# Kernel tuning notes

Measured on AMD Instinct MI355X. Metric: run time of the kernel, lower is better.

The kernel has to match this reference:

```python
import jax, jax.numpy as jnp
import numpy as np

SIGMA = 0.5          # kernel length_scale
SOFTNESS = 1.0       # softmax temperature scaling
B, F, J, M, U = 4096, 512, 16, 64, 512  # batch, feature, num_domains, domain_dim, units


def _gauss(sqdist):
    # ExponentiatedQuadratic with amplitude=1: exp(-||x-y||^2 / (2*sigma^2))
    return jnp.exp(-sqdist / (2.0 * SIGMA * SIGMA))


def setup_inputs() -> dict:
    key = jax.random.key(0)
    k1, k2, k3 = jax.random.split(key, 3)
    h = jax.random.normal(k1, (B, F), dtype=jnp.float32)
    # domain basis: keras RandomNormal() default stddev=0.05
    domains = 0.05 * jax.random.normal(k2, (J, M, F), dtype=jnp.float32)
    # W_domains: GlorotUniform over (M, U)
    limit = np.sqrt(6.0 / (M + U)).astype(np.float32)
    W = jax.random.uniform(k3, (J, M, U), dtype=jnp.float32, minval=-limit, maxval=limit)
    b = jnp.zeros((J, U), dtype=jnp.float32)
    return {"h": h, "domains": domains, "W": W, "b": b}


def reference(h, domains, W, b):
    # ---- kernel matrix between inputs and all domain bases: K[b,j,m] ----
    h2 = jnp.sum(h * h, axis=-1)                      # [B]
    d2 = jnp.sum(domains * domains, axis=-1)          # [J,M]
    cross = jnp.einsum('bf,jmf->bjm', h, domains)     # [B,J,M]
    K_hd = _gauss(h2[:, None, None] + d2[None] - 2.0 * cross)

    # ---- per-domain MMD: k(x,x) - 2*mean_m k(x,d_m) + mean_{m,m'} k(d_m,d_m') ----
    dd = d2[:, :, None] + d2[:, None, :] - 2.0 * jnp.einsum('jmf,jnf->jmn', domains, domains)
    k_dd_mean = jnp.mean(_gauss(dd), axis=(1, 2))     # [J]
    mmd = 1.0 - 2.0 * jnp.mean(K_hd, axis=2) + k_dd_mean[None, :]  # [B,J]

    # softmax over domains of -softness * mmd  -> domain probabilities [B,J]
    prob = jax.nn.softmax(-SOFTNESS * mmd, axis=1)

    # ---- representer outputs per domain: K(h, D_j) @ W_j + b_j ----
    out = jnp.einsum('bjm,jmu->bju', K_hd, W) + b[None]  # [B,J,U]

    # probability-weighted sum over domains
    return jnp.einsum('bj,bju->bu', prob, out)           # [B,U]
```

## Files before the change

kernel.cpp:

```cpp
#include <hip/hip_runtime.h>
#include <math.h>

typedef unsigned short ushort_t;
typedef __attribute__((ext_vector_type(8))) short bf16x8;
typedef __attribute__((ext_vector_type(4))) float f32x4;

#define B_SZ 4096
#define F_SZ 512
#define J_SZ 16
#define M_SZ 64
#define U_SZ 512
#define P_SZ 1024

__device__ __forceinline__ ushort_t f2bf(float f) {
    union { float f; unsigned int u; } v; v.f = f;
    unsigned int r = (v.u + 0x7FFFu + ((v.u >> 16) & 1u)) >> 16;
    return (ushort_t)r;
}

__device__ __forceinline__ void gload_lds16(const void* g, void* l) {
    __builtin_amdgcn_global_load_lds(
        (const __attribute__((address_space(1))) unsigned int*)g,
        (__attribute__((address_space(3))) unsigned int*)l, 16, 0, 0);
}

__global__ __launch_bounds__(256) void prep_kernel(const float* __restrict__ h,
                                                   const float* __restrict__ dom,
                                                   const float* __restrict__ W,
                                                   ushort_t* __restrict__ hbf,
                                                   ushort_t* __restrict__ dombf,
                                                   ushort_t* __restrict__ Wt,
                                                   float* __restrict__ h2,
                                                   float* __restrict__ d2,
                                                   float* __restrict__ Gpart) {
    const int bid = blockIdx.x;
    const int tid = threadIdx.x;

    if (bid < 1024) {
        int b = bid * 4 + (tid >> 6);
        int lane = tid & 63;
        const float4* row = (const float4*)(h + (size_t)b * F_SZ);
        ushort4* orow = (ushort4*)(hbf + (size_t)b * F_SZ);
        float s = 0.f;
        for (int i = lane; i < F_SZ / 4; i += 64) {
            float4 v = row[i];
            s += v.x * v.x + v.y * v.y + v.z * v.z + v.w * v.w;
            ushort4 o; o.x = f2bf(v.x); o.y = f2bf(v.y); o.z = f2bf(v.z); o.w = f2bf(v.w);
            orow[i] = o;
        }
        for (int off = 32; off; off >>= 1) s += __shfl_down(s, off);
        if (lane == 0) h2[b] = s;
    } else if (bid < 1280) {
        int p = (bid - 1024) * 4 + (tid >> 6);
        int lane = tid & 63;
        const float4* row = (const float4*)(dom + (size_t)p * F_SZ);
        ushort4* orow = (ushort4*)(dombf + (size_t)p * F_SZ);
        float s = 0.f;
        for (int i = lane; i < F_SZ / 4; i += 64) {
            float4 v = row[i];
            s += v.x * v.x + v.y * v.y + v.z * v.z + v.w * v.w;
            ushort4 o; o.x = f2bf(v.x); o.y = f2bf(v.y); o.z = f2bf(v.z); o.w = f2bf(v.w);
            orow[i] = o;
        }
        for (int off = 32; off; off >>= 1) s += __shfl_down(s, off);
        if (lane == 0) d2[p] = s;
    } else if (bid < 1344) {
        int idx = bid - 1280;
        int j = idx >> 2, kc = idx & 3;
        const float* base = dom + (size_t)j * M_SZ * F_SZ + kc * 128;
        __shared__ float As[32][68];
        int tx = tid & 15, ty = tid >> 4;
        float c[4][4] = {};
        for (int kk = 0; kk < 128; kk += 32) {
            for (int l = 0; l < 2; ++l) {
                int s = tid + l * 256;
                int r = s >> 3, c4 = (s & 7) << 2;
                float4 v = *(const float4*)&base[(size_t)r * F_SZ + kk + c4];
                As[c4 + 0][r] = v.x; As[c4 + 1][r] = v.y;
                As[c4 + 2][r] = v.z; As[c4 + 3][r] = v.w;
            }
            __syncthreads();
            for (int k = 0; k < 32; ++k) {
                float a[4], bv[4];
                for (int i = 0; i < 4; ++i) a[i] = As[k][ty * 4 + i];
                for (int i = 0; i < 4; ++i) bv[i] = As[k][tx * 4 + i];
                for (int i = 0; i < 4; ++i)
                    for (int l2 = 0; l2 < 4; ++l2) c[i][l2] += a[i] * bv[l2];
            }
            __syncthreads();
        }
        float* gout = Gpart + ((size_t)kc * 16 + j) * 4096;
        for (int i = 0; i < 4; ++i)
            for (int l2 = 0; l2 < 4; ++l2)
                gout[(ty * 4 + i) * 64 + tx * 4 + l2] = c[i][l2];
    } else {
        int idx = bid - 1344;
        int pt = (idx >> 3) * 64, ut = (idx & 7) * 64;
        __shared__ ushort_t T[64][72];
        for (int l = 0; l < 4; ++l) {
            int s = l * 256 + tid;
            int r = s >> 4, c4 = (s & 15) << 2;
            float4 v = *(const float4*)&W[(size_t)(pt + r) * U_SZ + ut + c4];
            T[c4 + 0][r] = f2bf(v.x); T[c4 + 1][r] = f2bf(v.y);
            T[c4 + 2][r] = f2bf(v.z); T[c4 + 3][r] = f2bf(v.w);
        }
        __syncthreads();
        for (int l = 0; l < 4; ++l) {
            int s = l * 256 + tid;
            int r2 = s >> 4, c4 = (s & 15) << 2;
            ushort4 o; o.x = T[r2][c4 + 0]; o.y = T[r2][c4 + 1];
            o.z = T[r2][c4 + 2]; o.w = T[r2][c4 + 3];
            *(ushort4*)&Wt[(size_t)(ut + r2) * P_SZ + pt + c4] = o;
        }
    }
}

__global__ __launch_bounds__(256) void kdd_reduce(const float* __restrict__ Gpart,
                                                  const float* __restrict__ d2,
                                                  float* __restrict__ kdd) {
    int j = blockIdx.x, tid = threadIdx.x;
    __shared__ float sd2[M_SZ];
    __shared__ float red[256];
    if (tid < M_SZ) sd2[tid] = d2[j * M_SZ + tid];
    __syncthreads();
    const float* g0 = Gpart + (size_t)(0 * 16 + j) * 4096;
    const float* g1 = Gpart + (size_t)(1 * 16 + j) * 4096;
    const float* g2 = Gpart + (size_t)(2 * 16 + j) * 4096;
    const float* g3 = Gpart + (size_t)(3 * 16 + j) * 4096;
    float acc = 0.f;
    for (int s = tid; s < 4096; s += 256) {
        float G = g0[s] + g1[s] + g2[s] + g3[s];
        int m = s >> 6, n = s & 63;
        acc += __expf(-2.f * (sd2[m] + sd2[n] - 2.f * G));
    }
    red[tid] = acc;
    __syncthreads();
    for (int off = 128; off; off >>= 1) {
        if (tid < off) red[tid] += red[tid + off];
        __syncthreads();
    }
    if (tid == 0) kdd[j] = red[0] * (1.f / 4096.f);
}

__global__ __launch_bounds__(256) void gemm1_mfma(const ushort_t* __restrict__ hbf,
                                                  const ushort_t* __restrict__ dombf,
                                                  const float* __restrict__ h2,
                                                  const float* __restrict__ d2,
                                                  ushort_t* __restrict__ Kbf,
                                                  float* __restrict__ sj) {
    __shared__ ushort_t smem[8448];
    short* As = (short*)smem;
    short* Bs = (short*)(smem + 2048);
    const int b0 = blockIdx.x * 64;
    const int p0 = blockIdx.y * 128;
    const int tid = threadIdx.x;
    const int wid = tid >> 6, lane = tid & 63;
    const int wm = wid >> 1, wn = wid & 1;
    const int lcol = lane & 15, quad = lane >> 4;

    f32x4 acc[2][4];
    for (int i = 0; i < 2; ++i)
        for (int n = 0; n < 4; ++n) acc[i][n] = (f32x4){0.f, 0.f, 0.f, 0.f};

    for (int kk = 0; kk < F_SZ; kk += 32) {
        {
            int row = tid >> 2, seg = tid & 3;
            gload_lds16(hbf + (size_t)(b0 + row) * F_SZ + kk + seg * 8, &As[tid * 8]);
        }
#pragma unroll
        for (int l = 0; l < 2; ++l) {
            int s = l * 256 + tid;
            int row = s >> 2, seg = s & 3;
            gload_lds16(dombf + (size_t)(p0 + row) * F_SZ + kk + seg * 8, &Bs[s * 8]);
        }
        __syncthreads();
        bf16x8 ar[2], br[4];
#pragma unroll
        for (int i = 0; i < 2; ++i)
            ar[i] = *(const bf16x8*)&As[(wm * 32 + i * 16 + lcol) * 32 + quad * 8];
#pragma unroll
        for (int n = 0; n < 4; ++n)
            br[n] = *(const bf16x8*)&Bs[(wn * 64 + n * 16 + lcol) * 32 + quad * 8];
#pragma unroll
        for (int i = 0; i < 2; ++i)
#pragma unroll
            for (int n = 0; n < 4; ++n)
                acc[i][n] = __builtin_amdgcn_mfma_f32_16x16x32_bf16(ar[i], br[n], acc[i][n], 0, 0, 0);
        __syncthreads();
    }

    const int jg = (p0 >> 6) + wn;
    float d2v[4];
#pragma unroll
    for (int n = 0; n < 4; ++n) d2v[n] = d2[p0 + wn * 64 + n * 16 + lcol];

    unsigned int stash[2][4][2];
#pragma unroll
    for (int i = 0; i < 2; ++i) {
#pragma unroll
        for (int r = 0; r < 4; ++r) {
            int b = b0 + wm * 32 + i * 16 + quad * 4 + r;
            float h2v = h2[b];
            float rs = 0.f;
            ushort_t kv[4];
#pragma unroll
            for (int n = 0; n < 4; ++n) {
                float sq = h2v + d2v[n] - 2.f * acc[i][n][r];
                float kvf = __expf(-2.f * sq);
                kv[n] = f2bf(kvf);
                rs += kvf;
            }
            stash[i][r][0] = (unsigned int)kv[0] | ((unsigned int)kv[1] << 16);
            stash[i][r][1] = (unsigned int)kv[2] | ((unsigned int)kv[3] << 16);
            rs += __shfl_xor(rs, 1);
            rs += __shfl_xor(rs, 2);
            rs += __shfl_xor(rs, 4);
            rs += __shfl_xor(rs, 8);
            if (lcol == 0) sj[(size_t)b * J_SZ + jg] = rs * (1.f / M_SZ);
        }
    }

    ushort_t* LDSC = smem;
#pragma unroll
    for (int i = 0; i < 2; ++i) {
#pragma unroll
        for (int r = 0; r < 4; ++r) {
            int row = wm * 32 + i * 16 + quad * 4 + r;
#pragma unroll
            for (int n = 0; n < 4; ++n) {
                ushort_t v = (ushort_t)(stash[i][r][n >> 1] >> ((n & 1) * 16));
                LDSC[row * 132 + wn * 64 + n * 16 + lcol] = v;
            }
        }
    }
    __syncthreads();
#pragma unroll
    for (int l = 0; l < 8; ++l) {
        int u = l * 256 + tid;
        int row = u >> 5, segc = (u & 31) * 4;
        ushort4 v = *(const ushort4*)&LDSC[row * 132 + segc];
        *(ushort4*)&Kbf[(size_t)(b0 + row) * P_SZ + p0 + segc] = v;
    }
}

__global__ __launch_bounds__(256) void gemm2_mfma(const ushort_t* __restrict__ Ks,
                                                  const ushort_t* __restrict__ Wt,
                                                  const float* __restrict__ sj,
                                                  const float* __restrict__ kdd,
                                                  const float* __restrict__ bias,
                                                  float* __restrict__ out) {
    __shared__ short As[64 * 32];
    __shared__ short Bs[64 * 32];
    __shared__ float probS[64 * 17];
    __shared__ float biasS[16 * 64];
    __shared__ float kddS[J_SZ];
    const int b0 = blockIdx.x * 64;
    const int u0 = blockIdx.y * 64;
    const int tid = threadIdx.x;
    const int wid = tid >> 6, lane = tid & 63;
    const int wm = wid >> 1, wn = wid & 1;
    const int lcol = lane & 15, quad = lane >> 4;

    if (tid < J_SZ) kddS[tid] = kdd[tid];
    {
        int rowj = tid >> 4, c4 = (tid & 15) << 2;
        *(float4*)&biasS[rowj * 64 + c4] = *(const float4*)&bias[(size_t)rowj * U_SZ + u0 + c4];
    }
    __syncthreads();
    if (tid < 64) {
        int b = b0 + tid;
        float lg[J_SZ], mx = -1e30f;
#pragma unroll
        for (int j = 0; j < J_SZ; ++j) {
            lg[j] = 2.f * sj[(size_t)b * J_SZ + j] - kddS[j] - 1.f;
            mx = fmaxf(mx, lg[j]);
        }
        float ssum = 0.f;
#pragma unroll
        for (int j = 0; j < J_SZ; ++j) { lg[j] = __expf(lg[j] - mx); ssum += lg[j]; }
        float inv = 1.f / ssum;
#pragma unroll
        for (int j = 0; j < J_SZ; ++j) probS[tid * 17 + j] = lg[j] * inv;
    }
    __syncthreads();

    f32x4 acc_tot[2][2], acc_cur[2][2];
    for (int i = 0; i < 2; ++i)
        for (int n = 0; n < 2; ++n) {
            acc_tot[i][n] = (f32x4){0.f, 0.f, 0.f, 0.f};
            acc_cur[i][n] = (f32x4){0.f, 0.f, 0.f, 0.f};
        }

    for (int jb = 0; jb < J_SZ; ++jb) {
        float pf[2][4];
#pragma unroll
        for (int i = 0; i < 2; ++i)
#pragma unroll
            for (int r = 0; r < 4; ++r)
                pf[i][r] = probS[(wm * 32 + i * 16 + quad * 4 + r) * 17 + jb];
#pragma unroll
        for (int s = 0; s < 2; ++s) {
            int kk = jb * 64 + s * 32;
            {
                int row = tid >> 2, seg = tid & 3;
                gload_lds16(Ks + (size_t)(b0 + row) * P_SZ + kk + seg * 8, &As[tid * 8]);
                gload_lds16(Wt + (size_t)(u0 + row) * P_SZ + kk + seg * 8, &Bs[tid * 8]);
            }
            __syncthreads();
            bf16x8 ar[2], br[2];
#pragma unroll
            for (int i = 0; i < 2; ++i)
                ar[i] = *(const bf16x8*)&As[(wm * 32 + i * 16 + lcol) * 32 + quad * 8];
#pragma unroll
            for (int n = 0; n < 2; ++n)
                br[n] = *(const bf16x8*)&Bs[(wn * 32 + n * 16 + lcol) * 32 + quad * 8];
#pragma unroll
            for (int i = 0; i < 2; ++i)
#pragma unroll
                for (int n = 0; n < 2; ++n)
                    acc_cur[i][n] = __builtin_amdgcn_mfma_f32_16x16x32_bf16(ar[i], br[n], acc_cur[i][n], 0, 0, 0);
            __syncthreads();
        }
#pragma unroll
        for (int i = 0; i < 2; ++i)
#pragma unroll
            for (int n = 0; n < 2; ++n) {
#pragma unroll
                for (int r = 0; r < 4; ++r)
                    acc_tot[i][n][r] += pf[i][r] * acc_cur[i][n][r];
                acc_cur[i][n] = (f32x4){0.f, 0.f, 0.f, 0.f};
            }
    }

    float bv[2][J_SZ];
#pragma unroll
    for (int n = 0; n < 2; ++n) {
        int col = wn * 32 + n * 16 + lcol;
#pragma unroll
        for (int j = 0; j < J_SZ; ++j) bv[n][j] = biasS[j * 64 + col];
    }
#pragma unroll
    for (int i = 0; i < 2; ++i) {
#pragma unroll
        for (int r = 0; r < 4; ++r) {
            int row = wm * 32 + i * 16 + quad * 4 + r;
            int b = b0 + row;
#pragma unroll
            for (int n = 0; n < 2; ++n) {
                float a = acc_tot[i][n][r];
#pragma unroll
                for (int j = 0; j < J_SZ; ++j) a += probS[row * 17 + j] * bv[n][j];
                out[(size_t)b * U_SZ + u0 + wn * 32 + n * 16 + lcol] = a;
            }
        }
    }
}

extern "C" void kernel_launch(void* const* d_in, const int* in_sizes, int n_in,
                              void* d_out, int out_size, void* d_ws, size_t ws_size,
                              hipStream_t stream) {
    const float* h    = (const float*)d_in[0];
    const float* dom  = (const float*)d_in[1];
    const float* W    = (const float*)d_in[2];
    const float* bias = (const float*)d_in[3];
    float* out = (float*)d_out;

    char* ws = (char*)d_ws;
    ushort_t* hbf   = (ushort_t*)ws;  ws += (size_t)B_SZ * F_SZ * 2;
    ushort_t* dombf = (ushort_t*)ws;  ws += (size_t)P_SZ * F_SZ * 2;
    ushort_t* Wt    = (ushort_t*)ws;  ws += (size_t)U_SZ * P_SZ * 2;
    ushort_t* Kbf   = (ushort_t*)ws;  ws += (size_t)B_SZ * P_SZ * 2;
    float* h2    = (float*)ws;  ws += B_SZ * 4;
    float* d2    = (float*)ws;  ws += P_SZ * 4;
    float* kdd   = (float*)ws;  ws += 64;
    float* sj    = (float*)ws;  ws += (size_t)B_SZ * J_SZ * 4;
    float* Gpart = (float*)ws;  ws += (size_t)4 * J_SZ * M_SZ * M_SZ * 4;

    prep_kernel<<<1472, 256, 0, stream>>>(h, dom, W, hbf, dombf, Wt, h2, d2, Gpart);
    kdd_reduce<<<J_SZ, 256, 0, stream>>>(Gpart, d2, kdd);
    gemm1_mfma<<<dim3(B_SZ / 64, P_SZ / 128), 256, 0, stream>>>(hbf, dombf, h2, d2, Kbf, sj);
    gemm2_mfma<<<dim3(B_SZ / 64, U_SZ / 64), 256, 0, stream>>>(Kbf, Wt, sj, kdd, bias, out);
}
```

Before: 111.2 us.

## Fuse kdd reduction into prep kernel and double K-tile depth in both GEMMs

The domain Gram/MMD self-term is now computed in one block per domain over the full feature dimension, with the exp-sum reduction done in place. This removes the separate kdd_reduce launch and the Gpart workspace round trip, at the cost of longer serial work in 16 blocks. Both MFMA GEMMs now stage 64-wide K tiles instead of 32, which halves the number of barrier-synchronised load/compute iterations and uses more LDS per block.

Result: slower. 124.3 us (+11.8%).

```diff
diff --git a/kernel.cpp b/kernel.cpp
--- a/kernel.cpp
+++ b/kernel.cpp
@@ -32,7 +32,7 @@
                                                    ushort_t* __restrict__ Wt,
                                                    float* __restrict__ h2,
                                                    float* __restrict__ d2,
-                                                   float* __restrict__ Gpart) {
+                                                   float* __restrict__ kdd) {
     const int bid = blockIdx.x;
     const int tid = threadIdx.x;
 
@@ -64,14 +64,15 @@
         }
         for (int off = 32; off; off >>= 1) s += __shfl_down(s, off);
         if (lane == 0) d2[p] = s;
-    } else if (bid < 1344) {
-        int idx = bid - 1280;
-        int j = idx >> 2, kc = idx & 3;
-        const float* base = dom + (size_t)j * M_SZ * F_SZ + kc * 128;
+    } else if (bid < 1296) {
+        int j = bid - 1280;
+        const float* base = dom + (size_t)j * M_SZ * F_SZ;
         __shared__ float As[32][68];
+        __shared__ float diag[M_SZ];
+        __shared__ float red[256];
         int tx = tid & 15, ty = tid >> 4;
         float c[4][4] = {};
-        for (int kk = 0; kk < 128; kk += 32) {
+        for (int kk = 0; kk < F_SZ; kk += 32) {
             for (int l = 0; l < 2; ++l) {
                 int s = tid + l * 256;
                 int r = s >> 3, c4 = (s & 7) << 2;
@@ -89,12 +90,26 @@
             }
             __syncthreads();
         }
-        float* gout = Gpart + ((size_t)kc * 16 + j) * 4096;
-        for (int i = 0; i < 4; ++i)
-            for (int l2 = 0; l2 < 4; ++l2)
-                gout[(ty * 4 + i) * 64 + tx * 4 + l2] = c[i][l2];
+        if (tx == ty)
+            for (int i = 0; i < 4; ++i) diag[ty * 4 + i] = c[i][i];
+        __syncthreads();
+        float acc = 0.f;
+        for (int i = 0; i < 4; ++i) {
+            float dm = diag[ty * 4 + i];
+            for (int l2 = 0; l2 < 4; ++l2) {
+                float sq = dm + diag[tx * 4 + l2] - 2.f * c[i][l2];
+                acc += __expf(-2.f * sq);
+            }
+        }
+        red[tid] = acc;
+        __syncthreads();
+        for (int off = 128; off; off >>= 1) {
+            if (tid < off) red[tid] += red[tid + off];
+            __syncthreads();
+        }
+        if (tid == 0) kdd[j] = red[0] * (1.f / 4096.f);
     } else {
-        int idx = bid - 1344;
+        int idx = bid - 1296;
         int pt = (idx >> 3) * 64, ut = (idx & 7) * 64;
         __shared__ ushort_t T[64][72];
         for (int l = 0; l < 4; ++l) {
@@ -113,33 +128,6 @@
             *(ushort4*)&Wt[(size_t)(ut + r2) * P_SZ + pt + c4] = o;
         }
     }
-}
-
-__global__ __launch_bounds__(256) void kdd_reduce(const float* __restrict__ Gpart,
-                                                  const float* __restrict__ d2,
-                                                  float* __restrict__ kdd) {
-    int j = blockIdx.x, tid = threadIdx.x;
-    __shared__ float sd2[M_SZ];
-    __shared__ float red[256];
-    if (tid < M_SZ) sd2[tid] = d2[j * M_SZ + tid];
-    __syncthreads();
-    const float* g0 = Gpart + (size_t)(0 * 16 + j) * 4096;
-    const float* g1 = Gpart + (size_t)(1 * 16 + j) * 4096;
-    const float* g2 = Gpart + (size_t)(2 * 16 + j) * 4096;
-    const float* g3 = Gpart + (size_t)(3 * 16 + j) * 4096;
-    float acc = 0.f;
-    for (int s = tid; s < 4096; s += 256) {
-        float G = g0[s] + g1[s] + g2[s] + g3[s];
-        int m = s >> 6, n = s & 63;
-        acc += __expf(-2.f * (sd2[m] + sd2[n] - 2.f * G));
-    }
-    red[tid] = acc;
-    __syncthreads();
-    for (int off = 128; off; off >>= 1) {
-        if (tid < off) red[tid] += red[tid + off];
-        __syncthreads();
-    }
-    if (tid == 0) kdd[j] = red[0] * (1.f / 4096.f);
 }
 
 __global__ __launch_bounds__(256) void gemm1_mfma(const ushort_t* __restrict__ hbf,
@@ -148,9 +136,9 @@
                                                   const float* __restrict__ d2,
                                                   ushort_t* __restrict__ Kbf,
                                                   float* __restrict__ sj) {
-    __shared__ ushort_t smem[8448];
+    __shared__ ushort_t smem[12288];
     short* As = (short*)smem;
-    short* Bs = (short*)(smem + 2048);
+    short* Bs = (short*)(smem + 4096);
     const int b0 = blockIdx.x * 64;
     const int p0 = blockIdx.y * 128;
     const int tid = threadIdx.x;
@@ -162,30 +150,38 @@
     for (int i = 0; i < 2; ++i)
         for (int n = 0; n < 4; ++n) acc[i][n] = (f32x4){0.f, 0.f, 0.f, 0.f};
 
-    for (int kk = 0; kk < F_SZ; kk += 32) {
-        {
-            int row = tid >> 2, seg = tid & 3;
-            gload_lds16(hbf + (size_t)(b0 + row) * F_SZ + kk + seg * 8, &As[tid * 8]);
-        }
+    for (int kk = 0; kk < F_SZ; kk += 64) {
 #pragma unroll
         for (int l = 0; l < 2; ++l) {
             int s = l * 256 + tid;
-            int row = s >> 2, seg = s & 3;
+            int row = s >> 3, seg = s & 7;
+            gload_lds16(hbf + (size_t)(b0 + row) * F_SZ + kk + seg * 8, &As[s * 8]);
+        }
+#pragma unroll
+        for (int l = 0; l < 4; ++l) {
+            int s = l * 256 + tid;
+            int row = s >> 3, seg = s & 7;
             gload_lds16(dombf + (size_t)(p0 + row) * F_SZ + kk + seg * 8, &Bs[s * 8]);
         }
         __syncthreads();
-        bf16x8 ar[2], br[4];
+        bf16x8 ar[2][2], br[4][2];
 #pragma unroll
         for (int i = 0; i < 2; ++i)
-            ar[i] = *(const bf16x8*)&As[(wm * 32 + i * 16 + lcol) * 32 + quad * 8];
+#pragma unroll
+            for (int ks = 0; ks < 2; ++ks)
+                ar[i][ks] = *(const bf16x8*)&As[(wm * 32 + i * 16 + lcol) * 64 + ks * 32 + quad * 8];
 #pragma unroll
         for (int n = 0; n < 4; ++n)
-            br[n] = *(const bf16x8*)&Bs[(wn * 64 + n * 16 + lcol) * 32 + quad * 8];
-#pragma unroll
-        for (int i = 0; i < 2; ++i)
-#pragma unroll
-            for (int n = 0; n < 4; ++n)
-                acc[i][n] = __builtin_amdgcn_mfma_f32_16x16x32_bf16(ar[i], br[n], acc[i][n], 0, 0, 0);
+#pragma unroll
+            for (int ks = 0; ks < 2; ++ks)
+                br[n][ks] = *(const bf16x8*)&Bs[(wn * 64 + n * 16 + lcol) * 64 + ks * 32 + quad * 8];
+#pragma unroll
+        for (int ks = 0; ks < 2; ++ks)
+#pragma unroll
+            for (int i = 0; i < 2; ++i)
+#pragma unroll
+                for (int n = 0; n < 4; ++n)
+                    acc[i][n] = __builtin_amdgcn_mfma_f32_16x16x32_bf16(ar[i][ks], br[n][ks], acc[i][n], 0, 0, 0);
         __syncthreads();
     }
 
@@ -249,8 +245,8 @@
                                                   const float* __restrict__ kdd,
                                                   const float* __restrict__ bias,
                                                   float* __restrict__ out) {
-    __shared__ short As[64 * 32];
-    __shared__ short Bs[64 * 32];
+    __shared__ short As[64 * 64];
+    __shared__ short Bs[64 * 64];
     __shared__ float probS[64 * 17];
     __shared__ float biasS[16 * 64];
     __shared__ float kddS[J_SZ];
@@ -284,52 +280,54 @@
     }
     __syncthreads();
 
-    f32x4 acc_tot[2][2], acc_cur[2][2];
+    f32x4 acc_tot[2][2];
     for (int i = 0; i < 2; ++i)
-        for (int n = 0; n < 2; ++n) {
-            acc_tot[i][n] = (f32x4){0.f, 0.f, 0.f, 0.f};
-            acc_cur[i][n] = (f32x4){0.f, 0.f, 0.f, 0.f};
-        }
+        for (int n = 0; n < 2; ++n) acc_tot[i][n] = (f32x4){0.f, 0.f, 0.f, 0.f};
 
     for (int jb = 0; jb < J_SZ; ++jb) {
-        float pf[2][4];
+        int kk = jb * 64;
+#pragma unroll
+        for (int l = 0; l < 2; ++l) {
+            int s = l * 256 + tid;
+            int row = s >> 3, seg = s & 7;
+            gload_lds16(Ks + (size_t)(b0 + row) * P_SZ + kk + seg * 8, &As[s * 8]);
+            gload_lds16(Wt + (size_t)(u0 + row) * P_SZ + kk + seg * 8, &Bs[s * 8]);
+        }
+        __syncthreads();
+        bf16x8 ar[2][2], br[2][2];
 #pragma unroll
         for (int i = 0; i < 2; ++i)
 #pragma unroll
-            for (int r = 0; r < 4; ++r)
-                pf[i][r] = probS[(wm * 32 + i * 16 + quad * 4 + r) * 17 + jb];
-#pragma unroll
-        for (int s = 0; s < 2; ++s) {
-            int kk = jb * 64 + s * 32;
-            {
-                int row = tid >> 2, seg = tid & 3;
-                gload_lds16(Ks + (size_t)(b0 + row) * P_SZ + kk + seg * 8, &As[tid * 8]);
-                gload_lds16(Wt + (size_t)(u0 + row) * P_SZ + kk + seg * 8, &Bs[tid * 8]);
-            }
-            __syncthreads();
-            bf16x8 ar[2], br[2];
+            for (int ks = 0; ks < 2; ++ks)
+                ar[i][ks] = *(const bf16x8*)&As[(wm * 32 + i * 16 + lcol) * 64 + ks * 32 + quad * 8];
+#pragma unroll
+        for (int n = 0; n < 2; ++n)
+#pragma unroll
+            for (int ks = 0; ks < 2; ++ks)
+                br[n][ks] = *(const bf16x8*)&Bs[(wn * 32 + n * 16 + lcol) * 64 + ks * 32 + quad * 8];
+        f32x4 acc_cur[2][2];
+#pragma unroll
+        for (int i = 0; i < 2; ++i)
+#pragma unroll
+            for (int n = 0; n < 2; ++n) acc_cur[i][n] = (f32x4){0.f, 0.f, 0.f, 0.f};
+#pragma unroll
+        for (int ks = 0; ks < 2; ++ks)
 #pragma unroll
             for (int i = 0; i < 2; ++i)
-                ar[i] = *(const bf16x8*)&As[(wm * 32 + i * 16 + lcol) * 32 + quad * 8];
-#pragma unroll
-            for (int n = 0; n < 2; ++n)
-                br[n] = *(const bf16x8*)&Bs[(wn * 32 + n * 16 + lcol) * 32 + quad * 8];
-#pragma unroll
-            for (int i = 0; i < 2; ++i)
 #pragma unroll
                 for (int n = 0; n < 2; ++n)
-                    acc_cur[i][n] = __builtin_amdgcn_mfma_f32_16x16x32_bf16(ar[i], br[n], acc_cur[i][n], 0, 0, 0);
-            __syncthreads();
-        }
-#pragma unroll
-        for (int i = 0; i < 2; ++i)
-#pragma unroll
-            for (int n = 0; n < 2; ++n) {
-#pragma unroll
-                for (int r = 0; r < 4; ++r)
-                    acc_tot[i][n][r] += pf[i][r] * acc_cur[i][n][r];
-                acc_cur[i][n] = (f32x4){0.f, 0.f, 0.f, 0.f};
-            }
+                    acc_cur[i][n] = __builtin_amdgcn_mfma_f32_16x16x32_bf16(ar[i][ks], br[n][ks], acc_cur[i][n], 0, 0, 0);
+        __syncthreads();
+#pragma unroll
+        for (int i = 0; i < 2; ++i) {
+#pragma unroll
+            for (int r = 0; r < 4; ++r) {
+                float pf = probS[(wm * 32 + i * 16 + quad * 4 + r) * 17 + jb];
+#pragma unroll
+                for (int n = 0; n < 2; ++n)
+                    acc_tot[i][n][r] += pf * acc_cur[i][n][r];
+            }
+        }
     }
 
     float bv[2][J_SZ];
@@ -370,14 +368,12 @@
     ushort_t* dombf = (ushort_t*)ws;  ws += (size_t)P_SZ * F_SZ * 2;
     ushort_t* Wt    = (ushort_t*)ws;  ws += (size_t)U_SZ * P_SZ * 2;
     ushort_t* Kbf   = (ushort_t*)ws;  ws += (size_t)B_SZ * P_SZ * 2;
-    float* h2    = (float*)ws;  ws += B_SZ * 4;
-    float* d2    = (float*)ws;  ws += P_SZ * 4;
-    float* kdd   = (float*)ws;  ws += 64;
-    float* sj    = (float*)ws;  ws += (size_t)B_SZ * J_SZ * 4;
-    float* Gpart = (float*)ws;  ws += (size_t)4 * J_SZ * M_SZ * M_SZ * 4;
-
-    prep_kernel<<<1472, 256, 0, stream>>>(h, dom, W, hbf, dombf, Wt, h2, d2, Gpart);
-    kdd_reduce<<<J_SZ, 256, 0, stream>>>(Gpart, d2, kdd);
+    float* h2  = (float*)ws;  ws += B_SZ * 4;
+    float* d2  = (float*)ws;  ws += P_SZ * 4;
+    float* kdd = (float*)ws;  ws += 64;
+    float* sj  = (float*)ws;  ws += (size_t)B_SZ * J_SZ * 4;
+
+    prep_kernel<<<1424, 256, 0, stream>>>(h, dom, W, hbf, dombf, Wt, h2, d2, kdd);
     gemm1_mfma<<<dim3(B_SZ / 64, P_SZ / 128), 256, 0, stream>>>(hbf, dombf, h2, d2, Kbf, sj);
     gemm2_mfma<<<dim3(B_SZ / 64, U_SZ / 64), 256, 0, stream>>>(Kbf, Wt, sj, kdd, bias, out);
 }
```
